# Optimization experiments

Hardware: AMD Instinct MI355X
Metric: run time of the kernel (lower is better)

## Reference

```python
import jax, jax.numpy as jnp
import numpy as np

B, T, H, A, V, L = 4096, 16, 768, 128, 16, 2

def setup_inputs() -> dict:
    key = jax.random.key(0)
    ks = jax.random.split(key, 8)
    s = 0.02
    return {
        "last_hidden": jax.random.normal(ks[0], (B, T, H), jnp.float32),
        "attention_mask": jnp.ones((B, T), jnp.int64),
        "variety_ids": jax.random.randint(ks[1], (B,), 0, V),
        "Wd": jax.random.normal(ks[2], (V, H, A), jnp.float32) * s,  # per-variety down-proj
        "bd": jnp.zeros((V, A), jnp.float32),
        "Wu": jax.random.normal(ks[3], (V, A, H), jnp.float32) * s,  # per-variety up-proj
        "bu": jnp.zeros((V, H), jnp.float32),
        "Wc": jax.random.normal(ks[4], (L, H), jnp.float32) * s,     # classifier
        "bc": jnp.zeros((L,), jnp.float32),
    }

def reference(last_hidden, attention_mask, variety_ids, Wd, bd, Wu, bu, Wc, bc):
    x = last_hidden[:, 0, :]                                   # (B,H) CLS token
    # Dense grouped adapter: run all V bottleneck adapters, then select per example.
    h = jax.nn.gelu(jnp.einsum('bh,vha->bva', x, Wd) + bd[None])   # (B,V,A)
    u = jnp.einsum('bva,vah->bvh', h, Wu) + bu[None]               # (B,V,H)
    sel = u[jnp.arange(x.shape[0]), variety_ids]                   # (B,H) routed output
    adapted = x + sel                                              # residual bottleneck adapter
    # dropout is identity at p=0.0 / eval
    return adapted @ Wc.T + bc                                     # (B,L) logits
```

## Files before the change

### kernel.cpp

```cpp
#include <hip/hip_runtime.h>
#include <hip/hip_bf16.h>

#define BB 4096
#define TT 16
#define HH 768
#define AA 128
#define VV 16
#define LL 2
#define KS 6

typedef __attribute__((ext_vector_type(8))) short short8v;
typedef __attribute__((ext_vector_type(4))) float float4v;

#define WS_OFFS 0
#define WS_ROWS 64
#define WS_WUC  4160
#define WS_BUC  8256
#define WS_WDP  8448
#define WS_ZBUF (8448 + (VV * KS * AA * 128) / 2)

__device__ __forceinline__ unsigned short f2bf(float f) {
    __hip_bfloat16 h = __float2bfloat16(f);
    return *reinterpret_cast<unsigned short*>(&h);
}

__device__ __forceinline__ float gelu_tanh(float z) {
    float y = 0.7978845608028654f * (z + 0.044715f * z * z * z);
    y = fminf(fmaxf(y, -15.f), 15.f);
    float e = __expf(2.f * y);
    float th = (e - 1.f) / (e + 1.f);
    return 0.5f * z * (1.f + th);
}

__global__ __launch_bounds__(256) void k_prep(
    const int*   __restrict__ variety_ids,
    const float* __restrict__ Wd,
    const float* __restrict__ Wu,
    const float* __restrict__ bu,
    const float* __restrict__ Wc,
    int* __restrict__ ws_i)
{
    __shared__ __align__(16) unsigned short Wds[128 * 136];
    __shared__ float sp0[256], sp1[256];
    __shared__ int hist[VV], hoff[VV + 1], hcur[VV];

    const int t = threadIdx.x;
    const int bid = blockIdx.x;
    unsigned short* wdp = (unsigned short*)(ws_i + WS_WDP);
    float* Wuc = (float*)(ws_i + WS_WUC);
    float* buc = (float*)(ws_i + WS_BUC);

    if (bid < 96) {
        const int v = bid / KS, ks = bid % KS;
        const float* wd = Wd + (size_t)v * HH * AA;
        const int ks0 = ks * 128;
        #pragma unroll
        for (int s = 0; s < 16; ++s) {
            int idx = t + s * 256;
            int hl  = idx >> 5;
            int a4  = idx & 31;
            float4 wv = *(const float4*)(wd + (size_t)(ks0 + hl) * AA + a4 * 4);
            Wds[(a4 * 4 + 0) * 136 + hl] = f2bf(wv.x);
            Wds[(a4 * 4 + 1) * 136 + hl] = f2bf(wv.y);
            Wds[(a4 * 4 + 2) * 136 + hl] = f2bf(wv.z);
            Wds[(a4 * 4 + 3) * 136 + hl] = f2bf(wv.w);
        }
        __syncthreads();
        unsigned short* dst = wdp + (size_t)(v * KS + ks) * AA * 128;
        #pragma unroll
        for (int s = 0; s < 8; ++s) {
            int G = t + s * 256;
            int a = G >> 4, g = G & 15;
            uint4 w = *(const uint4*)&Wds[a * 136 + g * 8];
            *(uint4*)&dst[a * 128 + g * 8] = w;
        }
    } else if (bid < 128) {
        const int v  = (bid - 96) >> 1;
        const int ah = (bid - 96) & 1;
        const int a  = ah * 64 + (t >> 2);
        const int q  = t & 3;
        const float* wu = Wu + (size_t)v * AA * HH + (size_t)a * HH;
        float s0 = 0.f, s1 = 0.f;
        #pragma unroll 4
        for (int h = q * 192; h < q * 192 + 192; h += 4) {
            float4 w  = *(const float4*)&wu[h];
            float4 c0 = *(const float4*)&Wc[h];
            float4 c1 = *(const float4*)&Wc[HH + h];
            s0 += w.x * c0.x + w.y * c0.y + w.z * c0.z + w.w * c0.w;
            s1 += w.x * c1.x + w.y * c1.y + w.z * c1.z + w.w * c1.w;
        }
        sp0[t] = s0; sp1[t] = s1;
        __syncthreads();
        if (t < 64) {
            float r0 = sp0[t * 4] + sp0[t * 4 + 1] + sp0[t * 4 + 2] + sp0[t * 4 + 3];
            float r1 = sp1[t * 4] + sp1[t * 4 + 1] + sp1[t * 4 + 2] + sp1[t * 4 + 3];
            int aa = ah * 64 + t;
            Wuc[(v * AA + aa) * LL + 0] = r0;
            Wuc[(v * AA + aa) * LL + 1] = r1;
        }
    } else if (bid == 128) {
        const int pair = t >> 3, seg = t & 7;
        const int v = pair >> 1, l = pair & 1;
        float s = 0.f;
        const float* bv = bu + (size_t)v * HH;
        for (int h = seg * 96; h < seg * 96 + 96; ++h) s += bv[h] * Wc[l * HH + h];
        sp0[t] = s;
        __syncthreads();
        if (t < 32) {
            float r = 0.f;
            #pragma unroll
            for (int i = 0; i < 8; ++i) r += sp0[t * 8 + i];
            buc[t] = r;
        }
    } else {
        if (t < VV) hist[t] = 0;
        __syncthreads();
        for (int b = t; b < BB; b += 256) atomicAdd(&hist[variety_ids[b]], 1);
        __syncthreads();
        if (t == 0) {
            int s = 0;
            for (int i = 0; i < VV; ++i) { hoff[i] = s; s += hist[i]; }
            hoff[VV] = s;
            for (int i = 0; i <= VV; ++i) ws_i[WS_OFFS + i] = hoff[i];
        }
        __syncthreads();
        if (t < VV) hcur[t] = hoff[t];
        __syncthreads();
        for (int b = t; b < BB; b += 256) {
            int v = variety_ids[b];
            int p = atomicAdd(&hcur[v], 1);
            ws_i[WS_ROWS + p] = b;
        }
    }
}

__global__ __launch_bounds__(256) void k_down_mfma(
    const float* __restrict__ last_hidden,
    const int*   __restrict__ ws_i,
    float* __restrict__ zbuf)
{
    __shared__ __align__(16) unsigned short Xs[128 * 136];
    __shared__ __align__(16) unsigned short Wds[128 * 136];
    __shared__ int srows[128];

    const int* offs = ws_i + WS_OFFS;
    const int* rows = ws_i + WS_ROWS;
    const unsigned short* wdp = (const unsigned short*)(ws_i + WS_WDP);
    const int t = threadIdx.x;

    const int ks = blockIdx.x % KS;
    const int rt = blockIdx.x / KS;
    int v = -1, tloc = 0, cnt = 0, obase = 0, acc_t = 0;
    for (int vv = 0; vv < VV; ++vv) {
        int c  = offs[vv + 1] - offs[vv];
        int nt = (c + 127) >> 7;
        if (rt < acc_t + nt) {
            v = vv; tloc = rt - acc_t;
            cnt = c - tloc * 128; if (cnt > 128) cnt = 128;
            obase = offs[vv];
            break;
        }
        acc_t += nt;
    }
    if (v < 0) return;

    if (t < 128) {
        int rr = t < cnt ? t : cnt - 1;
        srows[t] = rows[obase + tloc * 128 + rr];
    }
    __syncthreads();

    const int ks0 = ks * 128;
    #pragma unroll
    for (int s = 0; s < 16; ++s) {
        int idx = t + s * 256;
        int r   = idx >> 5;
        int k4  = idx & 31;
        const float* xr = last_hidden + (size_t)srows[r] * TT * HH + ks0 + k4 * 4;
        float4 xv = *(const float4*)xr;
        unsigned int p0 = (unsigned)f2bf(xv.x) | ((unsigned)f2bf(xv.y) << 16);
        unsigned int p1 = (unsigned)f2bf(xv.z) | ((unsigned)f2bf(xv.w) << 16);
        *(uint2*)&Xs[r * 136 + k4 * 4] = make_uint2(p0, p1);
    }
    {
        const unsigned short* wb = wdp + (size_t)(v * KS + ks) * AA * 128;
        #pragma unroll
        for (int s = 0; s < 8; ++s) {
            int G = t + s * 256;
            int a = G >> 4, g = G & 15;
            uint4 w = *(const uint4*)&wb[a * 128 + g * 8];
            *(uint4*)&Wds[a * 136 + g * 8] = w;
        }
    }
    __syncthreads();

    const int lane = t & 63;
    const int wv_  = t >> 6;
    const int wr = (wv_ >> 1) * 64, wc = (wv_ & 1) * 64;
    const int m = lane & 15, quad = lane >> 4;

    float4v acc[4][4];
    #pragma unroll
    for (int i = 0; i < 4; ++i)
        #pragma unroll
        for (int j = 0; j < 4; ++j)
            acc[i][j] = (float4v){0.f, 0.f, 0.f, 0.f};

    #pragma unroll
    for (int k0 = 0; k0 < 128; k0 += 32) {
        short8v af[4], bf[4];
        #pragma unroll
        for (int i = 0; i < 4; ++i)
            af[i] = *(const short8v*)&Xs[(wr + i * 16 + m) * 136 + k0 + quad * 8];
        #pragma unroll
        for (int j = 0; j < 4; ++j)
            bf[j] = *(const short8v*)&Wds[(wc + j * 16 + m) * 136 + k0 + quad * 8];
        #pragma unroll
        for (int i = 0; i < 4; ++i)
            #pragma unroll
            for (int j = 0; j < 4; ++j)
                acc[i][j] = __builtin_amdgcn_mfma_f32_16x16x32_bf16(af[i], bf[j], acc[i][j], 0, 0, 0);
    }

    float* zs = zbuf + (size_t)ks * BB * AA;
    #pragma unroll
    for (int i = 0; i < 4; ++i) {
        #pragma unroll
        for (int reg = 0; reg < 4; ++reg) {
            int r = wr + i * 16 + quad * 4 + reg;
            if (r < cnt) {
                size_t base = (size_t)(obase + tloc * 128 + r) * AA;
                #pragma unroll
                for (int j = 0; j < 4; ++j)
                    zs[base + wc + j * 16 + m] = acc[i][j][reg];
            }
        }
    }
}

__global__ __launch_bounds__(256) void k_combine(
    const float* __restrict__ last_hidden,
    const int*   __restrict__ ws_i,
    const float* __restrict__ bd,
    const float* __restrict__ Wc,
    const float* __restrict__ bc,
    const float* __restrict__ zbuf,
    float* __restrict__ out)
{
    const int* offs = ws_i + WS_OFFS;
    const int* rows = ws_i + WS_ROWS;
    const float* Wuc = (const float*)(ws_i + WS_WUC);
    const float* buc = (const float*)(ws_i + WS_BUC);

    const int pos  = blockIdx.x * 4 + (threadIdx.x >> 6);
    const int lane = threadIdx.x & 63;
    const int gr = rows[pos];
    int v = 0;
    for (int vv = 0; vv < VV; ++vv)
        if (pos >= offs[vv] && pos < offs[vv + 1]) v = vv;

    const int a0 = lane * 2;
    float z0 = 0.f, z1 = 0.f;
    #pragma unroll
    for (int ks = 0; ks < KS; ++ks) {
        float2 zz = *(const float2*)&zbuf[(size_t)ks * BB * AA + (size_t)pos * AA + a0];
        z0 += zz.x; z1 += zz.y;
    }
    z0 += bd[v * AA + a0];
    z1 += bd[v * AA + a0 + 1];
    float h0 = gelu_tanh(z0), h1 = gelu_tanh(z1);

    const float* wq = Wuc + (size_t)(v * AA + a0) * LL;
    float p0 = h0 * wq[0] + h1 * wq[2];
    float p1 = h0 * wq[1] + h1 * wq[3];

    const float* xr = last_hidden + (size_t)gr * TT * HH;
    #pragma unroll
    for (int s = 0; s < 12; ++s) {
        int h = lane + s * 64;
        float xv = xr[h];
        p0 += xv * Wc[h];
        p1 += xv * Wc[HH + h];
    }

    #pragma unroll
    for (int off = 32; off > 0; off >>= 1) {
        p0 += __shfl_down(p0, off);
        p1 += __shfl_down(p1, off);
    }
    if (lane == 0) {
        out[(size_t)gr * LL + 0] = p0 + bc[0] + buc[v * LL + 0];
        out[(size_t)gr * LL + 1] = p1 + bc[1] + buc[v * LL + 1];
    }
}

extern "C" void kernel_launch(void* const* d_in, const int* in_sizes, int n_in,
                              void* d_out, int out_size, void* d_ws, size_t ws_size,
                              hipStream_t stream) {
    const float* last_hidden = (const float*)d_in[0];
    const int*   variety_ids = (const int*)d_in[2];
    const float* Wd = (const float*)d_in[3];
    const float* bd = (const float*)d_in[4];
    const float* Wu = (const float*)d_in[5];
    const float* bu = (const float*)d_in[6];
    const float* Wc = (const float*)d_in[7];
    const float* bc = (const float*)d_in[8];
    float* out = (float*)d_out;

    int* ws_i = (int*)d_ws;
    float* zbuf = (float*)(ws_i + WS_ZBUF);

    k_prep<<<130, 256, 0, stream>>>(variety_ids, Wd, Wu, bu, Wc, ws_i);
    k_down_mfma<<<48 * KS, 256, 0, stream>>>(last_hidden, ws_i, zbuf);
    k_combine<<<BB / 4, 256, 0, stream>>>(last_hidden, ws_i, bd, Wc, bc, zbuf, out);
}
```

Baseline: 274.8 us.

## Fuse down-projection and combine into one kernel with in-block K loop

Replaces the split-K down-projection kernel plus its separate combine kernel with a single kernel. Each block handles a 64-row tile of one variety and loops over all six K chunks itself, so the fp32 partial-sum buffer and its global write and readback go away. GELU, the folded up-projection, and the classifier dot product (now an extra bf16 MFMA against Wc) are applied in the epilogue. The cost is a much smaller grid (79 blocks, each running a serial K loop with no overlap between loads and MFMA), and the x·Wc term now runs in bf16 instead of fp32.

```diff
diff --git a/kernel.cpp b/kernel.cpp
--- a/kernel.cpp
+++ b/kernel.cpp
@@ -7,7 +7,8 @@
 #define AA 128
 #define VV 16
 #define LL 2
-#define KS 6
+#define NCHUNK 6
+#define MT 64
 
 typedef __attribute__((ext_vector_type(8))) short short8v;
 typedef __attribute__((ext_vector_type(4))) float float4v;
@@ -17,7 +18,6 @@
 #define WS_WUC  4160
 #define WS_BUC  8256
 #define WS_WDP  8448
-#define WS_ZBUF (8448 + (VV * KS * AA * 128) / 2)
 
 __device__ __forceinline__ unsigned short f2bf(float f) {
     __hip_bfloat16 h = __float2bfloat16(f);
@@ -51,9 +51,9 @@
     float* buc = (float*)(ws_i + WS_BUC);
 
     if (bid < 96) {
-        const int v = bid / KS, ks = bid % KS;
+        const int v = bid / NCHUNK, kc = bid % NCHUNK;
         const float* wd = Wd + (size_t)v * HH * AA;
-        const int ks0 = ks * 128;
+        const int ks0 = kc * 128;
         #pragma unroll
         for (int s = 0; s < 16; ++s) {
             int idx = t + s * 256;
@@ -66,7 +66,7 @@
             Wds[(a4 * 4 + 3) * 136 + hl] = f2bf(wv.w);
         }
         __syncthreads();
-        unsigned short* dst = wdp + (size_t)(v * KS + ks) * AA * 128;
+        unsigned short* dst = wdp + (size_t)(v * NCHUNK + kc) * AA * 128;
         #pragma unroll
         for (int s = 0; s < 8; ++s) {
             int G = t + s * 256;
@@ -134,163 +134,176 @@
     }
 }
 
-__global__ __launch_bounds__(256) void k_down_mfma(
-    const float* __restrict__ last_hidden,
-    const int*   __restrict__ ws_i,
-    float* __restrict__ zbuf)
-{
-    __shared__ __align__(16) unsigned short Xs[128 * 136];
-    __shared__ __align__(16) unsigned short Wds[128 * 136];
-    __shared__ int srows[128];
-
-    const int* offs = ws_i + WS_OFFS;
-    const int* rows = ws_i + WS_ROWS;
-    const unsigned short* wdp = (const unsigned short*)(ws_i + WS_WDP);
-    const int t = threadIdx.x;
-
-    const int ks = blockIdx.x % KS;
-    const int rt = blockIdx.x / KS;
-    int v = -1, tloc = 0, cnt = 0, obase = 0, acc_t = 0;
-    for (int vv = 0; vv < VV; ++vv) {
-        int c  = offs[vv + 1] - offs[vv];
-        int nt = (c + 127) >> 7;
-        if (rt < acc_t + nt) {
-            v = vv; tloc = rt - acc_t;
-            cnt = c - tloc * 128; if (cnt > 128) cnt = 128;
-            obase = offs[vv];
-            break;
-        }
-        acc_t += nt;
-    }
-    if (v < 0) return;
-
-    if (t < 128) {
-        int rr = t < cnt ? t : cnt - 1;
-        srows[t] = rows[obase + tloc * 128 + rr];
-    }
-    __syncthreads();
-
-    const int ks0 = ks * 128;
-    #pragma unroll
-    for (int s = 0; s < 16; ++s) {
-        int idx = t + s * 256;
-        int r   = idx >> 5;
-        int k4  = idx & 31;
-        const float* xr = last_hidden + (size_t)srows[r] * TT * HH + ks0 + k4 * 4;
-        float4 xv = *(const float4*)xr;
-        unsigned int p0 = (unsigned)f2bf(xv.x) | ((unsigned)f2bf(xv.y) << 16);
-        unsigned int p1 = (unsigned)f2bf(xv.z) | ((unsigned)f2bf(xv.w) << 16);
-        *(uint2*)&Xs[r * 136 + k4 * 4] = make_uint2(p0, p1);
-    }
-    {
-        const unsigned short* wb = wdp + (size_t)(v * KS + ks) * AA * 128;
-        #pragma unroll
-        for (int s = 0; s < 8; ++s) {
-            int G = t + s * 256;
-            int a = G >> 4, g = G & 15;
-            uint4 w = *(const uint4*)&wb[a * 128 + g * 8];
-            *(uint4*)&Wds[a * 136 + g * 8] = w;
-        }
-    }
-    __syncthreads();
-
-    const int lane = t & 63;
-    const int wv_  = t >> 6;
-    const int wr = (wv_ >> 1) * 64, wc = (wv_ & 1) * 64;
-    const int m = lane & 15, quad = lane >> 4;
-
-    float4v acc[4][4];
-    #pragma unroll
-    for (int i = 0; i < 4; ++i)
-        #pragma unroll
-        for (int j = 0; j < 4; ++j)
-            acc[i][j] = (float4v){0.f, 0.f, 0.f, 0.f};
-
-    #pragma unroll
-    for (int k0 = 0; k0 < 128; k0 += 32) {
-        short8v af[4], bf[4];
-        #pragma unroll
-        for (int i = 0; i < 4; ++i)
-            af[i] = *(const short8v*)&Xs[(wr + i * 16 + m) * 136 + k0 + quad * 8];
-        #pragma unroll
-        for (int j = 0; j < 4; ++j)
-            bf[j] = *(const short8v*)&Wds[(wc + j * 16 + m) * 136 + k0 + quad * 8];
-        #pragma unroll
-        for (int i = 0; i < 4; ++i)
-            #pragma unroll
-            for (int j = 0; j < 4; ++j)
-                acc[i][j] = __builtin_amdgcn_mfma_f32_16x16x32_bf16(af[i], bf[j], acc[i][j], 0, 0, 0);
-    }
-
-    float* zs = zbuf + (size_t)ks * BB * AA;
-    #pragma unroll
-    for (int i = 0; i < 4; ++i) {
-        #pragma unroll
-        for (int reg = 0; reg < 4; ++reg) {
-            int r = wr + i * 16 + quad * 4 + reg;
-            if (r < cnt) {
-                size_t base = (size_t)(obase + tloc * 128 + r) * AA;
-                #pragma unroll
-                for (int j = 0; j < 4; ++j)
-                    zs[base + wc + j * 16 + m] = acc[i][j][reg];
-            }
-        }
-    }
-}
-
-__global__ __launch_bounds__(256) void k_combine(
+__global__ __launch_bounds__(256) void k_main(
     const float* __restrict__ last_hidden,
     const int*   __restrict__ ws_i,
     const float* __restrict__ bd,
     const float* __restrict__ Wc,
     const float* __restrict__ bc,
-    const float* __restrict__ zbuf,
     float* __restrict__ out)
 {
+    __shared__ __align__(16) unsigned short Xs[MT * 136];
+    __shared__ __align__(16) unsigned short Wds[128 * 136];
+    __shared__ __align__(16) unsigned short WcB[16 * 136];
+    __shared__ int srows[MT];
+    __shared__ float xc[MT * LL];
+
     const int* offs = ws_i + WS_OFFS;
     const int* rows = ws_i + WS_ROWS;
     const float* Wuc = (const float*)(ws_i + WS_WUC);
     const float* buc = (const float*)(ws_i + WS_BUC);
-
-    const int pos  = blockIdx.x * 4 + (threadIdx.x >> 6);
-    const int lane = threadIdx.x & 63;
-    const int gr = rows[pos];
-    int v = 0;
-    for (int vv = 0; vv < VV; ++vv)
-        if (pos >= offs[vv] && pos < offs[vv + 1]) v = vv;
-
-    const int a0 = lane * 2;
-    float z0 = 0.f, z1 = 0.f;
+    const unsigned short* wdp = (const unsigned short*)(ws_i + WS_WDP);
+    const int t = threadIdx.x;
+
+    const int rt = blockIdx.x;
+    int v = -1, tloc = 0, cnt = 0, obase = 0, acc_t = 0;
+    for (int vv = 0; vv < VV; ++vv) {
+        int c  = offs[vv + 1] - offs[vv];
+        int nt = (c + MT - 1) / MT;
+        if (rt < acc_t + nt) {
+            v = vv; tloc = rt - acc_t;
+            cnt = c - tloc * MT; if (cnt > MT) cnt = MT;
+            obase = offs[vv];
+            break;
+        }
+        acc_t += nt;
+    }
+    if (v < 0) return;
+
+    if (t < MT) {
+        int rr = t < cnt ? t : cnt - 1;
+        srows[t] = rows[obase + tloc * MT + rr];
+    }
+
+    const int lane = t & 63;
+    const int wv_  = t >> 6;
+    const int wr = (wv_ >> 1) * 32;
+    const int wc = (wv_ & 1) * 64;
+    const int m = lane & 15, quad = lane >> 4;
+
+    float4v acc[2][4];
+    float4v accx[2];
     #pragma unroll
-    for (int ks = 0; ks < KS; ++ks) {
-        float2 zz = *(const float2*)&zbuf[(size_t)ks * BB * AA + (size_t)pos * AA + a0];
-        z0 += zz.x; z1 += zz.y;
-    }
-    z0 += bd[v * AA + a0];
-    z1 += bd[v * AA + a0 + 1];
-    float h0 = gelu_tanh(z0), h1 = gelu_tanh(z1);
-
-    const float* wq = Wuc + (size_t)(v * AA + a0) * LL;
-    float p0 = h0 * wq[0] + h1 * wq[2];
-    float p1 = h0 * wq[1] + h1 * wq[3];
-
-    const float* xr = last_hidden + (size_t)gr * TT * HH;
-    #pragma unroll
-    for (int s = 0; s < 12; ++s) {
-        int h = lane + s * 64;
-        float xv = xr[h];
-        p0 += xv * Wc[h];
-        p1 += xv * Wc[HH + h];
-    }
-
-    #pragma unroll
-    for (int off = 32; off > 0; off >>= 1) {
-        p0 += __shfl_down(p0, off);
-        p1 += __shfl_down(p1, off);
-    }
-    if (lane == 0) {
-        out[(size_t)gr * LL + 0] = p0 + bc[0] + buc[v * LL + 0];
-        out[(size_t)gr * LL + 1] = p1 + bc[1] + buc[v * LL + 1];
+    for (int i = 0; i < 2; ++i) {
+        accx[i] = (float4v){0.f, 0.f, 0.f, 0.f};
+        #pragma unroll
+        for (int j = 0; j < 4; ++j)
+            acc[i][j] = (float4v){0.f, 0.f, 0.f, 0.f};
+    }
+
+    for (int kc = 0; kc < NCHUNK; ++kc) {
+        const int ks0 = kc * 128;
+        __syncthreads();
+        #pragma unroll
+        for (int s = 0; s < 8; ++s) {
+            int idx = t + s * 256;
+            int r   = idx >> 5;
+            int k4  = idx & 31;
+            const float* xr = last_hidden + (size_t)srows[r] * TT * HH + ks0 + k4 * 4;
+            float4 xv = *(const float4*)xr;
+            unsigned int p0 = (unsigned)f2bf(xv.x) | ((unsigned)f2bf(xv.y) << 16);
+            unsigned int p1 = (unsigned)f2bf(xv.z) | ((unsigned)f2bf(xv.w) << 16);
+            *(uint2*)&Xs[r * 136 + k4 * 4] = make_uint2(p0, p1);
+        }
+        {
+            const unsigned short* wb = wdp + (size_t)(v * NCHUNK + kc) * AA * 128;
+            #pragma unroll
+            for (int s = 0; s < 8; ++s) {
+                int G = t + s * 256;
+                int a = G >> 4, g = G & 15;
+                uint4 w = *(const uint4*)&wb[a * 128 + g * 8];
+                *(uint4*)&Wds[a * 136 + g * 8] = w;
+            }
+        }
+        {
+            int c = t >> 4, g = t & 15;
+            uint4 w = make_uint4(0u, 0u, 0u, 0u);
+            if (c < LL) {
+                const float* wcr = Wc + (size_t)c * HH + ks0 + g * 8;
+                float4 w0 = *(const float4*)wcr;
+                float4 w1 = *(const float4*)(wcr + 4);
+                w.x = (unsigned)f2bf(w0.x) | ((unsigned)f2bf(w0.y) << 16);
+                w.y = (unsigned)f2bf(w0.z) | ((unsigned)f2bf(w0.w) << 16);
+                w.z = (unsigned)f2bf(w1.x) | ((unsigned)f2bf(w1.y) << 16);
+                w.w = (unsigned)f2bf(w1.z) | ((unsigned)f2bf(w1.w) << 16);
+            }
+            *(uint4*)&WcB[c * 136 + g * 8] = w;
+        }
+        __syncthreads();
+
+        #pragma unroll
+        for (int k0 = 0; k0 < 128; k0 += 32) {
+            short8v af[2], bf[4];
+            #pragma unroll
+            for (int i = 0; i < 2; ++i)
+                af[i] = *(const short8v*)&Xs[(wr + i * 16 + m) * 136 + k0 + quad * 8];
+            #pragma unroll
+            for (int j = 0; j < 4; ++j)
+                bf[j] = *(const short8v*)&Wds[(wc + j * 16 + m) * 136 + k0 + quad * 8];
+            #pragma unroll
+            for (int i = 0; i < 2; ++i)
+                #pragma unroll
+                for (int j = 0; j < 4; ++j)
+                    acc[i][j] = __builtin_amdgcn_mfma_f32_16x16x32_bf16(af[i], bf[j], acc[i][j], 0, 0, 0);
+            if (wc == 0) {
+                short8v cf = *(const short8v*)&WcB[m * 136 + k0 + quad * 8];
+                #pragma unroll
+                for (int i = 0; i < 2; ++i)
+                    accx[i] = __builtin_amdgcn_mfma_f32_16x16x32_bf16(af[i], cf, accx[i], 0, 0, 0);
+            }
+        }
+    }
+
+    __syncthreads();
+    float* p_part = (float*)Wds;
+
+    {
+        const int wch = wc >> 6;
+        float bdv[4], w0v[4], w1v[4];
+        #pragma unroll
+        for (int j = 0; j < 4; ++j) {
+            int a = wc + j * 16 + m;
+            bdv[j] = bd[v * AA + a];
+            w0v[j] = Wuc[(v * AA + a) * LL + 0];
+            w1v[j] = Wuc[(v * AA + a) * LL + 1];
+        }
+        #pragma unroll
+        for (int i = 0; i < 2; ++i) {
+            #pragma unroll
+            for (int reg = 0; reg < 4; ++reg) {
+                int row = wr + i * 16 + quad * 4 + reg;
+                float p0 = 0.f, p1 = 0.f;
+                #pragma unroll
+                for (int j = 0; j < 4; ++j) {
+                    float h = gelu_tanh(acc[i][j][reg] + bdv[j]);
+                    p0 += h * w0v[j];
+                    p1 += h * w1v[j];
+                }
+                p_part[(row * LL + 0) * 32 + wch * 16 + m] = p0;
+                p_part[(row * LL + 1) * 32 + wch * 16 + m] = p1;
+            }
+        }
+        if (wc == 0 && m < LL) {
+            #pragma unroll
+            for (int i = 0; i < 2; ++i)
+                #pragma unroll
+                for (int reg = 0; reg < 4; ++reg) {
+                    int row = wr + i * 16 + quad * 4 + reg;
+                    xc[row * LL + m] = accx[i][reg];
+                }
+        }
+    }
+    __syncthreads();
+
+    if (t < MT * LL) {
+        int row = t >> 1, l = t & 1;
+        if (row < cnt) {
+            float s = 0.f;
+            #pragma unroll
+            for (int k = 0; k < 32; ++k) s += p_part[(row * LL + l) * 32 + k];
+            int gr = srows[row];
+            out[(size_t)gr * LL + l] = s + xc[row * LL + l] + buc[v * LL + l] + bc[l];
+        }
     }
 }
 
@@ -308,9 +321,7 @@
     float* out = (float*)d_out;
 
     int* ws_i = (int*)d_ws;
-    float* zbuf = (float*)(ws_i + WS_ZBUF);
 
     k_prep<<<130, 256, 0, stream>>>(variety_ids, Wd, Wu, bu, Wc, ws_i);
-    k_down_mfma<<<48 * KS, 256, 0, stream>>>(last_hidden, ws_i, zbuf);
-    k_combine<<<BB / 4, 256, 0, stream>>>(last_hidden, ws_i, bd, Wc, bc, zbuf, out);
-}
+    k_main<<<79, 256, 0, stream>>>(last_hidden, ws_i, bd, Wc, bc, out);
+}
```

After: 279.8 us. Within noise of the previous version (+1.8%).
